# Performance work log

Hardware: AMD Instinct MI355X
Metric: run time of the kernel (lower is better)

## Reference

```python
import jax, jax.numpy as jnp
import numpy as np

B, S, NCH, OUT = 16384, 256, 8, 2
EPS = 1e-5

def setup_inputs() -> dict:
    key = jax.random.key(0)
    ks = jax.random.split(key, 8)
    scale = 1.0 / np.sqrt(S)
    x = jax.random.normal(ks[0], (B, S, 2 * NCH), dtype=jnp.float32)
    h_0 = jnp.zeros((1,), dtype=jnp.float32)
    # per-channel complex linear weights, stacked: [n_channels, out=S, in=S]
    Wr = jax.random.normal(ks[1], (NCH, S, S), dtype=jnp.float32) * scale
    Wi = jax.random.normal(ks[2], (NCH, S, S), dtype=jnp.float32) * scale
    # final complex linear: [out=OUT//2, in=NCH*S]
    Wfr = jax.random.normal(ks[3], (OUT // 2, NCH * S), dtype=jnp.float32) / np.sqrt(NCH * S)
    Wfi = jax.random.normal(ks[4], (OUT // 2, NCH * S), dtype=jnp.float32) / np.sqrt(NCH * S)
    g_in = jnp.ones((2 * NCH,), dtype=jnp.float32)
    b_in = jnp.zeros((2 * NCH,), dtype=jnp.float32)
    g_out = jnp.ones((OUT,), dtype=jnp.float32)
    b_out = jnp.zeros((OUT,), dtype=jnp.float32)
    return {"x": x, "h_0": h_0, "Wr": Wr, "Wi": Wi, "Wfr": Wfr, "Wfi": Wfi,
            "g_in": g_in, "b_in": b_in, "g_out": g_out, "b_out": b_out}

def reference(x, h_0, Wr, Wi, Wfr, Wfi, g_in, b_in, g_out, b_out):
    # bn_in (training mode): x permuted to [B, 2n, S] in torch -> stats per feature over (B, S)
    mu = jnp.mean(x, axis=(0, 1))
    var = jnp.var(x, axis=(0, 1))  # biased, as torch uses for normalization
    xn = (x - mu) * jax.lax.rsqrt(var + EPS) * g_in + b_in  # [B, S, 2n]
    xi = xn[:, :, 0::2]  # [B, S, n] real parts
    xq = xn[:, :, 1::2]  # [B, S, n] imag parts
    # batched complex linear over channels: y[b,o,c] = sum_s x[b,s,c] W[c,o,s]
    cr = jnp.einsum('bsc,cos->boc', xi, Wr) - jnp.einsum('bsc,cos->boc', xq, Wi)
    ci = jnp.einsum('bsc,cos->boc', xq, Wr) + jnp.einsum('bsc,cos->boc', xi, Wi)
    amp2 = xi * xi + xq * xq  # [B, S, n]
    # channel blocks concatenated along last dim: channel-major ordering
    x_ii = jnp.transpose(amp2 * cr, (0, 2, 1)).reshape(B, NCH * S)
    x_qq = jnp.transpose(amp2 * ci, (0, 2, 1)).reshape(B, NCH * S)
    Cr = x_ii @ Wfr.T - x_qq @ Wfi.T  # [B, OUT//2]
    Ci = x_qq @ Wfr.T + x_ii @ Wfi.T
    y = jnp.concatenate([Cr, Ci], axis=-1)  # [B, OUT]
    mu2 = jnp.mean(y, axis=0)
    var2 = jnp.var(y, axis=0)
    return (y - mu2) * jax.lax.rsqrt(var2 + EPS) * g_out + b_out
```

## Files before the change

kernel.cpp:

```cpp
#include <hip/hip_runtime.h>
#include <stdint.h>

#define B_N   16384
#define S_N   256
#define NCH   8
#define P_N   (B_N * S_N)
#define EPS_F 1e-5f

typedef float  f32x4  __attribute__((ext_vector_type(4)));
typedef __bf16 bf16x8 __attribute__((ext_vector_type(8)));
typedef unsigned int u32x4 __attribute__((ext_vector_type(4)));
typedef unsigned int u32x2 __attribute__((ext_vector_type(2)));

static __device__ __forceinline__ unsigned short f2bf(float f) {
  union { float f; unsigned u; } v; v.f = f;
  unsigned u = v.u;
  u += 0x7fffu + ((u >> 16) & 1u);
  return (unsigned short)(u >> 16);
}
static __device__ __forceinline__ float bf2f(unsigned short h) {
  union { unsigned u; float f; } v; v.u = ((unsigned)h) << 16;
  return v.f;
}

typedef const __attribute__((address_space(1))) unsigned int* gas1_t;
typedef __attribute__((address_space(3))) unsigned int* las3_t;
static __device__ __forceinline__ void gl16(const void* g, void* l) {
  __builtin_amdgcn_global_load_lds((gas1_t)(uintptr_t)g,
                                   (las3_t)(unsigned int)(uintptr_t)l, 16, 0, 0);
}

__global__ __launch_bounds__(256) void pass1_kernel(
    const float* __restrict__ x, unsigned short* __restrict__ xplan,
    float* __restrict__ partials)
{
  __shared__ float ps[4][32];
  const int t = threadIdx.x;
  const int q = t & 3;
  const int pg = t >> 2;
  float s[4] = {0.f,0.f,0.f,0.f}, ss[4] = {0.f,0.f,0.f,0.f};
  const f32x4* xv = (const f32x4*)x;

  for (int it = 0; it < 4; ++it) {
    size_t p0 = ((size_t)blockIdx.x * 4 + it) * 512 + (size_t)pg * 8;
    f32x4 v[8];
    #pragma unroll
    for (int j = 0; j < 8; ++j) v[j] = xv[(p0 + j) * 4 + q];
    #pragma unroll
    for (int j = 0; j < 8; ++j)
      #pragma unroll
      for (int k = 0; k < 4; ++k) { s[k] += v[j][k]; ss[k] += v[j][k] * v[j][k]; }
    #pragma unroll
    for (int j2 = 0; j2 < 4; ++j2) {
      u32x4 w;
      #pragma unroll
      for (int k = 0; k < 4; ++k)
        w[k] = (unsigned)f2bf(v[2*k][j2]) | ((unsigned)f2bf(v[2*k+1][j2]) << 16);
      *(u32x4*)(xplan + (size_t)(q * 4 + j2) * P_N + p0) = w;
    }
  }

  #pragma unroll
  for (int off = 32; off >= 4; off >>= 1) {
    #pragma unroll
    for (int k = 0; k < 4; ++k) { s[k] += __shfl_down(s[k], off); ss[k] += __shfl_down(ss[k], off); }
  }
  const int lane = t & 63, wid = t >> 6;
  if (lane < 4) {
    #pragma unroll
    for (int k = 0; k < 4; ++k) {
      ps[wid][lane * 4 + k]      = s[k];
      ps[wid][16 + lane * 4 + k] = ss[k];
    }
  }
  __syncthreads();
  if (t < 32)
    partials[blockIdx.x * 32 + t] = ps[0][t] + ps[1][t] + ps[2][t] + ps[3][t];
}

__global__ __launch_bounds__(1024) void finalize_kernel(
    const float* __restrict__ partials, const float* __restrict__ g_in,
    const float* __restrict__ b_in, float* __restrict__ AC)
{
  __shared__ float acc[32][32];
  const int t = threadIdx.x;
  const int v = t & 31, chunk = t >> 5;
  float s = 0.f;
  for (int i = 0; i < 64; ++i)
    s += partials[(size_t)(chunk * 64 + i) * 32 + v];
  acc[chunk][v] = s;
  __syncthreads();
  if (t < 32) {
    float tot = 0.f;
    #pragma unroll
    for (int k = 0; k < 32; ++k) tot += acc[k][t];
    acc[0][t] = tot;
  }
  __syncthreads();
  if (t < 16) {
    float n = (float)P_N;
    float mu  = acc[0][t] / n;
    float var = acc[0][16 + t] / n - mu * mu;
    float A = g_in[t] * rsqrtf(var + EPS_F);
    AC[t] = A;
    AC[16 + t] = b_in[t] - mu * A;
  }
}

__global__ __launch_bounds__(256) void wprep_kernel(
    const float* __restrict__ Wr, const float* __restrict__ Wi,
    unsigned short* __restrict__ wr_bf, unsigned short* __restrict__ wi_bf,
    float* __restrict__ RWr, float* __restrict__ RWi)
{
  __shared__ float sr[4], si[4];
  const int row = blockIdx.x, t = threadIdx.x;
  const size_t idx = (size_t)row * 256 + t;
  float vr = Wr[idx], vi = Wi[idx];
  wr_bf[idx] = f2bf(vr);
  wi_bf[idx] = f2bf(vi);
  float rr = vr, ri = vi;
  #pragma unroll
  for (int off = 32; off >= 1; off >>= 1) { rr += __shfl_down(rr, off); ri += __shfl_down(ri, off); }
  if ((t & 63) == 0) { sr[t >> 6] = rr; si[t >> 6] = ri; }
  __syncthreads();
  if (t == 0) {
    RWr[row] = sr[0] + sr[1] + sr[2] + sr[3];
    RWi[row] = si[0] + si[1] + si[2] + si[3];
  }
}

__global__ __launch_bounds__(256) void kterm_kernel(
    const float* __restrict__ AC, const float* __restrict__ RWr, const float* __restrict__ RWi,
    float* __restrict__ Kr, float* __restrict__ Ki)
{
  int idx = blockIdx.x * 256 + threadIdx.x;
  int c = idx >> 8;
  float Ci_ = AC[16 + 2*c], Cq_ = AC[16 + 2*c + 1];
  Kr[idx] = Ci_ * RWr[idx] - Cq_ * RWi[idx];
  Ki[idx] = Cq_ * RWr[idx] + Ci_ * RWi[idx];
}

static __device__ __forceinline__ void issue_w(
    const unsigned short* __restrict__ wr_bf, const unsigned short* __restrict__ wi_bf,
    int c, int u, char* wbuf, int t)
{
  const int oh = u >> 3, c32 = u & 7;
  #pragma unroll
  for (int i = 0; i < 4; ++i) {
    const int L = i * 4096 + t * 16;
    const int row = i * 32 + (t >> 3);
    const int ds_ = (t & 7) ^ (row & 7);
    const unsigned short* wb = (ds_ & 4) ? wi_bf : wr_bf;
    const char* g = (const char*)(wb + (size_t)(c * 256 + oh * 128 + row) * 256
                                     + c32 * 32 + (ds_ & 3) * 8);
    gl16(g, wbuf + L);
  }
}

__global__ __launch_bounds__(256, 2) void main_kernel(
    const unsigned short* __restrict__ xplan,
    const unsigned short* __restrict__ wr_bf,
    const unsigned short* __restrict__ wi_bf,
    const float* __restrict__ AC,
    const float* __restrict__ Kr, const float* __restrict__ Ki,
    const float* __restrict__ Wfr, const float* __restrict__ Wfi,
    float* __restrict__ y)
{
  __shared__ char Xlds[32768];
  __shared__ char Wlds[2][16384];
  __shared__ float red[4][32][2];

  const int t = threadIdx.x;
  const int wid = t >> 6, lane = t & 63;
  const int col = lane & 15, kg = lane >> 4;
  const int b0 = blockIdx.x * 32;

  float pCr[2][4], pCi[2][4];
  #pragma unroll
  for (int m = 0; m < 2; ++m)
    #pragma unroll
    for (int r = 0; r < 4; ++r) { pCr[m][r] = 0.f; pCi[m][r] = 0.f; }

  int cur = 0;
  for (int c = 0; c < NCH; ++c) {
    #pragma unroll
    for (int i = 0; i < 8; ++i) {
      const int plane = i >> 2, si = i & 3;
      const int L = plane * 16384 + si * 4096 + t * 16;
      const int row = si * 8 + (t >> 5);
      const int gd = (t & 31) ^ (row & 7);
      const char* g = (const char*)xplan
          + (((size_t)(2 * c + plane) * P_N + (size_t)(b0 + row) * 256) << 1) + (gd << 4);
      gl16(g, &Xlds[L]);
    }
    issue_w(wr_bf, wi_bf, c, 0, &Wlds[cur][0], t);
    __syncthreads();

    for (int oh = 0; oh < 2; ++oh) {
      f32x4 Srr[2][2], Sqi[2][2], Sqr[2][2], Sii[2][2];
      #pragma unroll
      for (int m = 0; m < 2; ++m)
        #pragma unroll
        for (int n = 0; n < 2; ++n) {
          Srr[m][n] = (f32x4){0.f,0.f,0.f,0.f};
          Sqi[m][n] = (f32x4){0.f,0.f,0.f,0.f};
          Sqr[m][n] = (f32x4){0.f,0.f,0.f,0.f};
          Sii[m][n] = (f32x4){0.f,0.f,0.f,0.f};
        }
      #pragma unroll
      for (int t7 = 0; t7 < 8; ++t7) {
        const int u = oh * 8 + t7;
        if (u < 15) issue_w(wr_bf, wi_bf, c, u + 1, &Wlds[cur ^ 1][0], t);

        const int axo = ((((u & 7) * 4 + kg) ^ (col & 7)) << 4);
        const char* XiP = Xlds;
        const char* XqP = Xlds + 16384;
        bf16x8 ari0 = *(const bf16x8*)(XiP + col * 512 + axo);
        bf16x8 ari1 = *(const bf16x8*)(XiP + (16 + col) * 512 + axo);
        bf16x8 aqi0 = *(const bf16x8*)(XqP + col * 512 + axo);
        bf16x8 aqi1 = *(const bf16x8*)(XqP + (16 + col) * 512 + axo);
        const char* Wb = &Wlds[cur][0];
        #pragma unroll
        for (int nf = 0; nf < 2; ++nf) {
          const int r = wid * 32 + nf * 16 + col;
          bf16x8 br = *(const bf16x8*)(Wb + r * 128 + (((kg    ) ^ (r & 7)) << 4));
          bf16x8 bi = *(const bf16x8*)(Wb + r * 128 + (((kg + 4) ^ (r & 7)) << 4));
          Srr[0][nf] = __builtin_amdgcn_mfma_f32_16x16x32_bf16(ari0, br, Srr[0][nf], 0,0,0);
          Srr[1][nf] = __builtin_amdgcn_mfma_f32_16x16x32_bf16(ari1, br, Srr[1][nf], 0,0,0);
          Sqr[0][nf] = __builtin_amdgcn_mfma_f32_16x16x32_bf16(aqi0, br, Sqr[0][nf], 0,0,0);
          Sqr[1][nf] = __builtin_amdgcn_mfma_f32_16x16x32_bf16(aqi1, br, Sqr[1][nf], 0,0,0);
          Sii[0][nf] = __builtin_amdgcn_mfma_f32_16x16x32_bf16(ari0, bi, Sii[0][nf], 0,0,0);
          Sii[1][nf] = __builtin_amdgcn_mfma_f32_16x16x32_bf16(ari1, bi, Sii[1][nf], 0,0,0);
          Sqi[0][nf] = __builtin_amdgcn_mfma_f32_16x16x32_bf16(aqi0, bi, Sqi[0][nf], 0,0,0);
          Sqi[1][nf] = __builtin_amdgcn_mfma_f32_16x16x32_bf16(aqi1, bi, Sqi[1][nf], 0,0,0);
        }
        __syncthreads();
        cur ^= 1;
      }

      const float Ai_ = AC[2*c],      Aq_ = AC[2*c + 1];
      const float Cin = AC[16 + 2*c], Cqn = AC[16 + 2*c + 1];
      #pragma unroll
      for (int nf = 0; nf < 2; ++nf) {
        const int o = oh * 128 + wid * 32 + nf * 16 + col;
        const int gidx = c * 256 + o;
        const float kr = Kr[gidx], ki = Ki[gidx];
        const float wfr = Wfr[gidx], wfi = Wfi[gidx];
        const int og = o >> 3, ob = (o & 7) * 2;
        #pragma unroll
        for (int mf = 0; mf < 2; ++mf) {
          const int bl = mf * 16 + kg * 4;
          #pragma unroll
          for (int r = 0; r < 4; ++r) {
            const int row = bl + r;
            const int sb = row * 512 + ((og ^ (row & 7)) << 4) + ob;
            float xiv = Ai_ * bf2f(*(const unsigned short*)(Xlds + sb)) + Cin;
            float xqv = Aq_ * bf2f(*(const unsigned short*)(Xlds + 16384 + sb)) + Cqn;
            float cr = Ai_ * Srr[mf][nf][r] - Aq_ * Sqi[mf][nf][r] + kr;
            float ci = Aq_ * Sqr[mf][nf][r] + Ai_ * Sii[mf][nf][r] + ki;
            float amp2 = xiv * xiv + xqv * xqv;
            pCr[mf][r] += amp2 * (cr * wfr - ci * wfi);
            pCi[mf][r] += amp2 * (ci * wfr + cr * wfi);
          }
        }
      }
    }
    __syncthreads();
  }

  #pragma unroll
  for (int off = 1; off < 16; off <<= 1) {
    #pragma unroll
    for (int m = 0; m < 2; ++m)
      #pragma unroll
      for (int r = 0; r < 4; ++r) {
        pCr[m][r] += __shfl_xor(pCr[m][r], off);
        pCi[m][r] += __shfl_xor(pCi[m][r], off);
      }
  }
  if (col == 0) {
    #pragma unroll
    for (int m = 0; m < 2; ++m)
      #pragma unroll
      for (int r = 0; r < 4; ++r) {
        red[wid][m*16 + kg*4 + r][0] = pCr[m][r];
        red[wid][m*16 + kg*4 + r][1] = pCi[m][r];
      }
  }
  __syncthreads();
  if (t < 64) {
    int bl = t >> 1, cc = t & 1;
    float v = red[0][bl][cc] + red[1][bl][cc] + red[2][bl][cc] + red[3][bl][cc];
    y[(size_t)(b0 + bl) * 2 + cc] = v;
  }
}

__global__ __launch_bounds__(1024) void ln_kernel(
    const float* __restrict__ y, const float* __restrict__ g_out, const float* __restrict__ b_out,
    float* __restrict__ out)
{
  __shared__ float wsum[16][4];
  __shared__ float st[4];
  const int t = threadIdx.x;
  float s0 = 0.f, q0 = 0.f, s1 = 0.f, q1 = 0.f;
  for (int r = t; r < B_N; r += 1024) {
    float v0 = y[2*r], v1 = y[2*r + 1];
    s0 += v0; q0 += v0 * v0;
    s1 += v1; q1 += v1 * v1;
  }
  #pragma unroll
  for (int off = 32; off >= 1; off >>= 1) {
    s0 += __shfl_down(s0, off); q0 += __shfl_down(q0, off);
    s1 += __shfl_down(s1, off); q1 += __shfl_down(q1, off);
  }
  if ((t & 63) == 0) { int w = t >> 6; wsum[w][0]=s0; wsum[w][1]=q0; wsum[w][2]=s1; wsum[w][3]=q1; }
  __syncthreads();
  if (t == 0) {
    float S0=0.f,Q0=0.f,S1=0.f,Q1=0.f;
    for (int w = 0; w < 16; ++w) { S0+=wsum[w][0]; Q0+=wsum[w][1]; S1+=wsum[w][2]; Q1+=wsum[w][3]; }
    float n = (float)B_N;
    float mu0 = S0 / n, var0 = Q0 / n - mu0 * mu0;
    float mu1 = S1 / n, var1 = Q1 / n - mu1 * mu1;
    st[0] = mu0; st[1] = rsqrtf(var0 + EPS_F);
    st[2] = mu1; st[3] = rsqrtf(var1 + EPS_F);
  }
  __syncthreads();
  float g0 = g_out[0], g1 = g_out[1], bo0 = b_out[0], bo1 = b_out[1];
  float mu0 = st[0], rs0 = st[1], mu1 = st[2], rs1 = st[3];
  for (int r = t; r < B_N; r += 1024) {
    out[2*r]     = (y[2*r]     - mu0) * rs0 * g0 + bo0;
    out[2*r + 1] = (y[2*r + 1] - mu1) * rs1 * g1 + bo1;
  }
}

extern "C" void kernel_launch(void* const* d_in, const int* in_sizes, int n_in,
                              void* d_out, int out_size, void* d_ws, size_t ws_size,
                              hipStream_t stream) {
  (void)in_sizes; (void)n_in; (void)out_size; (void)ws_size;
  const float* x    = (const float*)d_in[0];
  const float* Wr   = (const float*)d_in[2];
  const float* Wi   = (const float*)d_in[3];
  const float* Wfr  = (const float*)d_in[4];
  const float* Wfi  = (const float*)d_in[5];
  const float* g_in = (const float*)d_in[6];
  const float* b_in = (const float*)d_in[7];
  const float* g_out= (const float*)d_in[8];
  const float* b_out= (const float*)d_in[9];
  float* out = (float*)d_out;

  char* ws = (char*)d_ws;
  float* AC    = (float*)(ws + 128);
  float* RWr   = (float*)(ws + 256);
  float* RWi   = (float*)(ws + 256 + 8192);
  float* Kr    = (float*)(ws + 256 + 16384);
  float* Ki    = (float*)(ws + 256 + 24576);
  float* y     = (float*)(ws + 33024);
  float* partials = (float*)(ws + 164096);
  unsigned short* wr_bf = (unsigned short*)(ws + 164096);
  unsigned short* wi_bf = (unsigned short*)(ws + 164096 + 1048576);
  unsigned short* xplan = (unsigned short*)(ws + 2261248);

  pass1_kernel<<<2048, 256, 0, stream>>>(x, xplan, partials);
  finalize_kernel<<<1, 1024, 0, stream>>>(partials, g_in, b_in, AC);
  wprep_kernel<<<2048, 256, 0, stream>>>(Wr, Wi, wr_bf, wi_bf, RWr, RWi);
  kterm_kernel<<<8, 256, 0, stream>>>(AC, RWr, RWi, Kr, Ki);
  main_kernel<<<B_N / 32, 256, 0, stream>>>(xplan, wr_bf, wi_bf, AC, Kr, Ki, Wfr, Wfi, y);
  ln_kernel<<<1, 1024, 0, stream>>>(y, g_out, b_out, out);
}
```

Measured before the change: 206.9 us.

## Triple-buffer weight tiles with explicit vmcnt waits and single barrier per step

```diff
diff --git a/kernel.cpp b/kernel.cpp
--- a/kernel.cpp
+++ b/kernel.cpp
@@ -157,6 +157,21 @@
   }
 }
 
+static __device__ __forceinline__ void issue_x(
+    const unsigned short* __restrict__ xplan, int c, int b0, char* xlds, int t)
+{
+  #pragma unroll
+  for (int i = 0; i < 8; ++i) {
+    const int plane = i >> 2, si = i & 3;
+    const int L = plane * 16384 + si * 4096 + t * 16;
+    const int row = si * 8 + (t >> 5);
+    const int gd = (t & 31) ^ (row & 7);
+    const char* g = (const char*)xplan
+        + (((size_t)(2 * c + plane) * P_N + (size_t)(b0 + row) * 256) << 1) + (gd << 4);
+    gl16(g, xlds + L);
+  }
+}
+
 __global__ __launch_bounds__(256, 2) void main_kernel(
     const unsigned short* __restrict__ xplan,
     const unsigned short* __restrict__ wr_bf,
@@ -167,8 +182,8 @@
     float* __restrict__ y)
 {
   __shared__ char Xlds[32768];
-  __shared__ char Wlds[2][16384];
-  __shared__ float red[4][32][2];
+  __shared__ char Wlds[49152];
+  float (*red)[32][2] = (float(*)[32][2])Wlds;
 
   const int t = threadIdx.x;
   const int wid = t >> 6, lane = t & 63;
@@ -181,20 +196,11 @@
     #pragma unroll
     for (int r = 0; r < 4; ++r) { pCr[m][r] = 0.f; pCi[m][r] = 0.f; }
 
-  int cur = 0;
   for (int c = 0; c < NCH; ++c) {
-    #pragma unroll
-    for (int i = 0; i < 8; ++i) {
-      const int plane = i >> 2, si = i & 3;
-      const int L = plane * 16384 + si * 4096 + t * 16;
-      const int row = si * 8 + (t >> 5);
-      const int gd = (t & 31) ^ (row & 7);
-      const char* g = (const char*)xplan
-          + (((size_t)(2 * c + plane) * P_N + (size_t)(b0 + row) * 256) << 1) + (gd << 4);
-      gl16(g, &Xlds[L]);
-    }
-    issue_w(wr_bf, wi_bf, c, 0, &Wlds[cur][0], t);
-    __syncthreads();
+    __builtin_amdgcn_s_barrier();
+    issue_x(xplan, c, b0, Xlds, t);
+    issue_w(wr_bf, wi_bf, c, 0, Wlds, t);
+    int wsel = 0;
 
     for (int oh = 0; oh < 2; ++oh) {
       f32x4 Srr[2][2], Sqi[2][2], Sqr[2][2], Sii[2][2];
@@ -210,16 +216,22 @@
       #pragma unroll
       for (int t7 = 0; t7 < 8; ++t7) {
         const int u = oh * 8 + t7;
-        if (u < 15) issue_w(wr_bf, wi_bf, c, u + 1, &Wlds[cur ^ 1][0], t);
-
-        const int axo = ((((u & 7) * 4 + kg) ^ (col & 7)) << 4);
-        const char* XiP = Xlds;
-        const char* XqP = Xlds + 16384;
-        bf16x8 ari0 = *(const bf16x8*)(XiP + col * 512 + axo);
-        bf16x8 ari1 = *(const bf16x8*)(XiP + (16 + col) * 512 + axo);
-        bf16x8 aqi0 = *(const bf16x8*)(XqP + col * 512 + axo);
-        bf16x8 aqi1 = *(const bf16x8*)(XqP + (16 + col) * 512 + axo);
-        const char* Wb = &Wlds[cur][0];
+        const int nsel = (wsel == 2) ? 0 : wsel + 1;
+        if (u < 15) {
+          issue_w(wr_bf, wi_bf, c, u + 1, Wlds + nsel * 16384, t);
+          asm volatile("s_waitcnt vmcnt(4)" ::: "memory");
+        } else {
+          asm volatile("s_waitcnt vmcnt(0)" ::: "memory");
+        }
+        __builtin_amdgcn_s_barrier();
+        __builtin_amdgcn_sched_barrier(0);
+
+        const int axo = (((t7 * 4 + kg) ^ (col & 7)) << 4);
+        bf16x8 ari0 = *(const bf16x8*)(Xlds + col * 512 + axo);
+        bf16x8 ari1 = *(const bf16x8*)(Xlds + (16 + col) * 512 + axo);
+        bf16x8 aqi0 = *(const bf16x8*)(Xlds + 16384 + col * 512 + axo);
+        bf16x8 aqi1 = *(const bf16x8*)(Xlds + 16384 + (16 + col) * 512 + axo);
+        const char* Wb = Wlds + wsel * 16384;
         #pragma unroll
         for (int nf = 0; nf < 2; ++nf) {
           const int r = wid * 32 + nf * 16 + col;
@@ -234,8 +246,8 @@
           Sqi[0][nf] = __builtin_amdgcn_mfma_f32_16x16x32_bf16(aqi0, bi, Sqi[0][nf], 0,0,0);
           Sqi[1][nf] = __builtin_amdgcn_mfma_f32_16x16x32_bf16(aqi1, bi, Sqi[1][nf], 0,0,0);
         }
-        __syncthreads();
-        cur ^= 1;
+        __builtin_amdgcn_sched_barrier(0);
+        wsel = nsel;
       }
 
       const float Ai_ = AC[2*c],      Aq_ = AC[2*c + 1];
@@ -265,7 +277,6 @@
         }
       }
     }
-    __syncthreads();
   }
 
   #pragma unroll
@@ -278,6 +289,7 @@
         pCi[m][r] += __shfl_xor(pCi[m][r], off);
       }
   }
+  __syncthreads();
   if (col == 0) {
     #pragma unroll
     for (int m = 0; m < 2; ++m)
```

Measured after the change: 201.8 us. -2.5%, faster.

## Load pre-packed bf16 weights directly to registers and switch to 32x32x16 MFMA

Applied to the files above, without the earlier changes.

```diff
diff --git a/kernel.cpp b/kernel.cpp
--- a/kernel.cpp
+++ b/kernel.cpp
@@ -8,6 +8,7 @@
 #define EPS_F 1e-5f
 
 typedef float  f32x4  __attribute__((ext_vector_type(4)));
+typedef float  f32x16 __attribute__((ext_vector_type(16)));
 typedef __bf16 bf16x8 __attribute__((ext_vector_type(8)));
 typedef unsigned int u32x4 __attribute__((ext_vector_type(4)));
 typedef unsigned int u32x2 __attribute__((ext_vector_type(2)));
@@ -109,15 +110,17 @@
 
 __global__ __launch_bounds__(256) void wprep_kernel(
     const float* __restrict__ Wr, const float* __restrict__ Wi,
-    unsigned short* __restrict__ wr_bf, unsigned short* __restrict__ wi_bf,
+    unsigned short* __restrict__ wrp, unsigned short* __restrict__ wip,
     float* __restrict__ RWr, float* __restrict__ RWi)
 {
   __shared__ float sr[4], si[4];
   const int row = blockIdx.x, t = threadIdx.x;
+  const int c = row >> 8, o = row & 255;
   const size_t idx = (size_t)row * 256 + t;
   float vr = Wr[idx], vi = Wi[idx];
-  wr_bf[idx] = f2bf(vr);
-  wi_bf[idx] = f2bf(vi);
+  const size_t widx = ((size_t)((c * 16 + (t >> 4)) * 2 + ((t >> 3) & 1)) * 256 + o) * 8 + (t & 7);
+  wrp[widx] = f2bf(vr);
+  wip[widx] = f2bf(vi);
   float rr = vr, ri = vi;
   #pragma unroll
   for (int off = 32; off >= 1; off >>= 1) { rr += __shfl_down(rr, off); ri += __shfl_down(ri, off); }
@@ -140,152 +143,126 @@
   Ki[idx] = Cq_ * RWr[idx] + Ci_ * RWi[idx];
 }
 
-static __device__ __forceinline__ void issue_w(
-    const unsigned short* __restrict__ wr_bf, const unsigned short* __restrict__ wi_bf,
-    int c, int u, char* wbuf, int t)
-{
-  const int oh = u >> 3, c32 = u & 7;
-  #pragma unroll
-  for (int i = 0; i < 4; ++i) {
-    const int L = i * 4096 + t * 16;
-    const int row = i * 32 + (t >> 3);
-    const int ds_ = (t & 7) ^ (row & 7);
-    const unsigned short* wb = (ds_ & 4) ? wi_bf : wr_bf;
-    const char* g = (const char*)(wb + (size_t)(c * 256 + oh * 128 + row) * 256
-                                     + c32 * 32 + (ds_ & 3) * 8);
-    gl16(g, wbuf + L);
-  }
-}
-
-__global__ __launch_bounds__(256, 2) void main_kernel(
+static __device__ __forceinline__ void issue_x(
+    const unsigned short* __restrict__ xplan, int c, int b0, char* xlds, int t)
+{
+  #pragma unroll
+  for (int i = 0; i < 8; ++i) {
+    const int plane = i >> 2, si = i & 3;
+    const int L = plane * 16384 + si * 4096 + t * 16;
+    const int row = si * 8 + (t >> 5);
+    const int gd = (t & 31) ^ (row & 7);
+    const char* g = (const char*)xplan
+        + (((size_t)(2 * c + plane) * P_N + (size_t)(b0 + row) * 256) << 1) + (gd << 4);
+    gl16(g, xlds + L);
+  }
+}
+
+__global__ __launch_bounds__(256, 3) void main_kernel(
     const unsigned short* __restrict__ xplan,
-    const unsigned short* __restrict__ wr_bf,
-    const unsigned short* __restrict__ wi_bf,
+    const unsigned short* __restrict__ wrp,
+    const unsigned short* __restrict__ wip,
     const float* __restrict__ AC,
     const float* __restrict__ Kr, const float* __restrict__ Ki,
     const float* __restrict__ Wfr, const float* __restrict__ Wfi,
     float* __restrict__ y)
 {
   __shared__ char Xlds[32768];
-  __shared__ char Wlds[2][16384];
   __shared__ float red[4][32][2];
 
   const int t = threadIdx.x;
   const int wid = t >> 6, lane = t & 63;
-  const int col = lane & 15, kg = lane >> 4;
+  const int ocol = lane & 31, khalf = lane >> 5;
+  const int arow = ocol;
+  const int arow7 = arow & 7;
   const int b0 = blockIdx.x * 32;
 
-  float pCr[2][4], pCi[2][4];
-  #pragma unroll
-  for (int m = 0; m < 2; ++m)
-    #pragma unroll
-    for (int r = 0; r < 4; ++r) { pCr[m][r] = 0.f; pCi[m][r] = 0.f; }
-
-  int cur = 0;
+  float pC0[16], pC1[16];
+  #pragma unroll
+  for (int i = 0; i < 16; ++i) { pC0[i] = 0.f; pC1[i] = 0.f; }
+
+  const char* XiB = Xlds + arow * 512;
+  const char* XqB = Xlds + 16384 + arow * 512;
+
   for (int c = 0; c < NCH; ++c) {
-    #pragma unroll
-    for (int i = 0; i < 8; ++i) {
-      const int plane = i >> 2, si = i & 3;
-      const int L = plane * 16384 + si * 4096 + t * 16;
-      const int row = si * 8 + (t >> 5);
-      const int gd = (t & 31) ^ (row & 7);
-      const char* g = (const char*)xplan
-          + (((size_t)(2 * c + plane) * P_N + (size_t)(b0 + row) * 256) << 1) + (gd << 4);
-      gl16(g, &Xlds[L]);
-    }
-    issue_w(wr_bf, wi_bf, c, 0, &Wlds[cur][0], t);
     __syncthreads();
+    issue_x(xplan, c, b0, Xlds, t);
+    __syncthreads();
+
+    const float Ai_ = AC[2*c],      Aq_ = AC[2*c + 1];
+    const float Cin = AC[16 + 2*c], Cqn = AC[16 + 2*c + 1];
 
     for (int oh = 0; oh < 2; ++oh) {
-      f32x4 Srr[2][2], Sqi[2][2], Sqr[2][2], Sii[2][2];
+      const int o = oh * 128 + wid * 32 + ocol;
+      const char* brP = (const char*)wrp + (size_t)c * 131072 + khalf * 4096 + o * 16;
+      const char* biP = (const char*)wip + (size_t)c * 131072 + khalf * 4096 + o * 16;
+
+      f32x16 Srr, Sqr, Sii, Sqi;
       #pragma unroll
-      for (int m = 0; m < 2; ++m)
-        #pragma unroll
-        for (int n = 0; n < 2; ++n) {
-          Srr[m][n] = (f32x4){0.f,0.f,0.f,0.f};
-          Sqi[m][n] = (f32x4){0.f,0.f,0.f,0.f};
-          Sqr[m][n] = (f32x4){0.f,0.f,0.f,0.f};
-          Sii[m][n] = (f32x4){0.f,0.f,0.f,0.f};
+      for (int i = 0; i < 16; ++i) { Srr[i]=0.f; Sqr[i]=0.f; Sii[i]=0.f; Sqi[i]=0.f; }
+
+      bf16x8 brA = *(const bf16x8*)(brP);
+      bf16x8 biA = *(const bf16x8*)(biP);
+      #pragma unroll 1
+      for (int u = 0; u < 16; u += 2) {
+        bf16x8 brB = *(const bf16x8*)(brP + (u + 1) * 8192);
+        bf16x8 biB = *(const bf16x8*)(biP + (u + 1) * 8192);
+        {
+          const int axo = ((u * 2 + khalf) ^ arow7) << 4;
+          bf16x8 axi = *(const bf16x8*)(XiB + axo);
+          bf16x8 axq = *(const bf16x8*)(XqB + axo);
+          Srr = __builtin_amdgcn_mfma_f32_32x32x16_bf16(axi, brA, Srr, 0,0,0);
+          Sqr = __builtin_amdgcn_mfma_f32_32x32x16_bf16(axq, brA, Sqr, 0,0,0);
+          Sii = __builtin_amdgcn_mfma_f32_32x32x16_bf16(axi, biA, Sii, 0,0,0);
+          Sqi = __builtin_amdgcn_mfma_f32_32x32x16_bf16(axq, biA, Sqi, 0,0,0);
         }
-      #pragma unroll
-      for (int t7 = 0; t7 < 8; ++t7) {
-        const int u = oh * 8 + t7;
-        if (u < 15) issue_w(wr_bf, wi_bf, c, u + 1, &Wlds[cur ^ 1][0], t);
-
-        const int axo = ((((u & 7) * 4 + kg) ^ (col & 7)) << 4);
-        const char* XiP = Xlds;
-        const char* XqP = Xlds + 16384;
-        bf16x8 ari0 = *(const bf16x8*)(XiP + col * 512 + axo);
-        bf16x8 ari1 = *(const bf16x8*)(XiP + (16 + col) * 512 + axo);
-        bf16x8 aqi0 = *(const bf16x8*)(XqP + col * 512 + axo);
-        bf16x8 aqi1 = *(const bf16x8*)(XqP + (16 + col) * 512 + axo);
-        const char* Wb = &Wlds[cur][0];
-        #pragma unroll
-        for (int nf = 0; nf < 2; ++nf) {
-          const int r = wid * 32 + nf * 16 + col;
-          bf16x8 br = *(const bf16x8*)(Wb + r * 128 + (((kg    ) ^ (r & 7)) << 4));
-          bf16x8 bi = *(const bf16x8*)(Wb + r * 128 + (((kg + 4) ^ (r & 7)) << 4));
-          Srr[0][nf] = __builtin_amdgcn_mfma_f32_16x16x32_bf16(ari0, br, Srr[0][nf], 0,0,0);
-          Srr[1][nf] = __builtin_amdgcn_mfma_f32_16x16x32_bf16(ari1, br, Srr[1][nf], 0,0,0);
-          Sqr[0][nf] = __builtin_amdgcn_mfma_f32_16x16x32_bf16(aqi0, br, Sqr[0][nf], 0,0,0);
-          Sqr[1][nf] = __builtin_amdgcn_mfma_f32_16x16x32_bf16(aqi1, br, Sqr[1][nf], 0,0,0);
-          Sii[0][nf] = __builtin_amdgcn_mfma_f32_16x16x32_bf16(ari0, bi, Sii[0][nf], 0,0,0);
-          Sii[1][nf] = __builtin_amdgcn_mfma_f32_16x16x32_bf16(ari1, bi, Sii[1][nf], 0,0,0);
-          Sqi[0][nf] = __builtin_amdgcn_mfma_f32_16x16x32_bf16(aqi0, bi, Sqi[0][nf], 0,0,0);
-          Sqi[1][nf] = __builtin_amdgcn_mfma_f32_16x16x32_bf16(aqi1, bi, Sqi[1][nf], 0,0,0);
-        }
-        __syncthreads();
-        cur ^= 1;
-      }
-
-      const float Ai_ = AC[2*c],      Aq_ = AC[2*c + 1];
-      const float Cin = AC[16 + 2*c], Cqn = AC[16 + 2*c + 1];
-      #pragma unroll
-      for (int nf = 0; nf < 2; ++nf) {
-        const int o = oh * 128 + wid * 32 + nf * 16 + col;
-        const int gidx = c * 256 + o;
-        const float kr = Kr[gidx], ki = Ki[gidx];
-        const float wfr = Wfr[gidx], wfi = Wfi[gidx];
-        const int og = o >> 3, ob = (o & 7) * 2;
-        #pragma unroll
-        for (int mf = 0; mf < 2; ++mf) {
-          const int bl = mf * 16 + kg * 4;
-          #pragma unroll
-          for (int r = 0; r < 4; ++r) {
-            const int row = bl + r;
-            const int sb = row * 512 + ((og ^ (row & 7)) << 4) + ob;
-            float xiv = Ai_ * bf2f(*(const unsigned short*)(Xlds + sb)) + Cin;
-            float xqv = Aq_ * bf2f(*(const unsigned short*)(Xlds + 16384 + sb)) + Cqn;
-            float cr = Ai_ * Srr[mf][nf][r] - Aq_ * Sqi[mf][nf][r] + kr;
-            float ci = Aq_ * Sqr[mf][nf][r] + Ai_ * Sii[mf][nf][r] + ki;
-            float amp2 = xiv * xiv + xqv * xqv;
-            pCr[mf][r] += amp2 * (cr * wfr - ci * wfi);
-            pCi[mf][r] += amp2 * (ci * wfr + cr * wfi);
-          }
+        brA = *(const bf16x8*)(brP + (u + 2) * 8192);
+        biA = *(const bf16x8*)(biP + (u + 2) * 8192);
+        {
+          const int axo = (((u + 1) * 2 + khalf) ^ arow7) << 4;
+          bf16x8 axi = *(const bf16x8*)(XiB + axo);
+          bf16x8 axq = *(const bf16x8*)(XqB + axo);
+          Srr = __builtin_amdgcn_mfma_f32_32x32x16_bf16(axi, brB, Srr, 0,0,0);
+          Sqr = __builtin_amdgcn_mfma_f32_32x32x16_bf16(axq, brB, Sqr, 0,0,0);
+          Sii = __builtin_amdgcn_mfma_f32_32x32x16_bf16(axi, biB, Sii, 0,0,0);
+          Sqi = __builtin_amdgcn_mfma_f32_32x32x16_bf16(axq, biB, Sqi, 0,0,0);
         }
       }
-    }
-    __syncthreads();
-  }
-
-  #pragma unroll
-  for (int off = 1; off < 16; off <<= 1) {
-    #pragma unroll
-    for (int m = 0; m < 2; ++m)
+
+      const int gidx = c * 256 + o;
+      const float kr = Kr[gidx], ki = Ki[gidx];
+      const float wfr = Wfr[gidx], wfi = Wfi[gidx];
+      const int og = o >> 3, ob = (o & 7) * 2;
       #pragma unroll
-      for (int r = 0; r < 4; ++r) {
-        pCr[m][r] += __shfl_xor(pCr[m][r], off);
-        pCi[m][r] += __shfl_xor(pCi[m][r], off);
+      for (int q = 0; q < 16; ++q) {
+        const int brow = (q & 3) + 8 * (q >> 2) + 4 * khalf;
+        const int sb = brow * 512 + ((og ^ (brow & 7)) << 4) + ob;
+        float xiv = Ai_ * bf2f(*(const unsigned short*)(Xlds + sb)) + Cin;
+        float xqv = Aq_ * bf2f(*(const unsigned short*)(Xlds + 16384 + sb)) + Cqn;
+        float cr = Ai_ * Srr[q] - Aq_ * Sqi[q] + kr;
+        float ci = Aq_ * Sqr[q] + Ai_ * Sii[q] + ki;
+        float amp2 = xiv * xiv + xqv * xqv;
+        pC0[q] += amp2 * (cr * wfr - ci * wfi);
+        pC1[q] += amp2 * (ci * wfr + cr * wfi);
       }
-  }
-  if (col == 0) {
-    #pragma unroll
-    for (int m = 0; m < 2; ++m)
-      #pragma unroll
-      for (int r = 0; r < 4; ++r) {
-        red[wid][m*16 + kg*4 + r][0] = pCr[m][r];
-        red[wid][m*16 + kg*4 + r][1] = pCi[m][r];
-      }
+    }
+  }
+
+  #pragma unroll
+  for (int off = 1; off < 32; off <<= 1) {
+    #pragma unroll
+    for (int q = 0; q < 16; ++q) {
+      pC0[q] += __shfl_xor(pC0[q], off);
+      pC1[q] += __shfl_xor(pC1[q], off);
+    }
+  }
+  if ((lane & 31) == 0) {
+    #pragma unroll
+    for (int q = 0; q < 16; ++q) {
+      const int brow = (q & 3) + 8 * (q >> 2) + 4 * khalf;
+      red[wid][brow][0] = pC0[q];
+      red[wid][brow][1] = pC1[q];
+    }
   }
   __syncthreads();
   if (t < 64) {
@@ -356,14 +333,14 @@
   float* Ki    = (float*)(ws + 256 + 24576);
   float* y     = (float*)(ws + 33024);
   float* partials = (float*)(ws + 164096);
-  unsigned short* wr_bf = (unsigned short*)(ws + 164096);
-  unsigned short* wi_bf = (unsigned short*)(ws + 164096 + 1048576);
+  unsigned short* wrp = (unsigned short*)(ws + 164096);
+  unsigned short* wip = (unsigned short*)(ws + 164096 + 1048576);
   unsigned short* xplan = (unsigned short*)(ws + 2261248);
 
   pass1_kernel<<<2048, 256, 0, stream>>>(x, xplan, partials);
   finalize_kernel<<<1, 1024, 0, stream>>>(partials, g_in, b_in, AC);
-  wprep_kernel<<<2048, 256, 0, stream>>>(Wr, Wi, wr_bf, wi_bf, RWr, RWi);
+  wprep_kernel<<<2048, 256, 0, stream>>>(Wr, Wi, wrp, wip, RWr, RWi);
   kterm_kernel<<<8, 256, 0, stream>>>(AC, RWr, RWi, Kr, Ki);
-  main_kernel<<<B_N / 32, 256, 0, stream>>>(xplan, wr_bf, wi_bf, AC, Kr, Ki, Wfr, Wfi, y);
+  main_kernel<<<B_N / 32, 256, 0, stream>>>(xplan, wrp, wip, AC, Kr, Ki, Wfr, Wfi, y);
   ln_kernel<<<1, 1024, 0, stream>>>(y, g_out, b_out, out);
 }
```

Result: slower. 431.7 us (+108.6%).
